# Optimization experiments

Hardware: AMD Instinct MI355X
Metric: run time of the kernel (lower is better)

Reference implementation:

```python
import jax, jax.numpy as jnp
import numpy as np
from jax import lax

B, N, IN_DIM = 8, 196, 2048
C = 256          # conv_channels / subspace dim
G = 1            # relation_glimpse


def _dilated_conv(x, w, b, dil):
    # x: [B,N,N,Cin], w: [3,3,Cin,Cout], SAME padding, rhs dilation per source
    y = lax.conv_general_dilated(x, w, window_strides=(1, 1), padding='SAME',
                                 rhs_dilation=dil,
                                 dimension_numbers=('NHWC', 'HWIO', 'NHWC'))
    return y + b


def _rel_map(X):
    # X: [B,N,N,G] -> symmetric add, move glimpse to axis 1, softmax over N*N
    Xs = X + jnp.transpose(X, (0, 2, 1, 3))          # [B,N,N,G]
    m = jnp.transpose(Xs, (0, 3, 2, 1))              # [B,G,N,N]
    bsz, g, n, _ = m.shape
    m = jax.nn.softmax(m.reshape(bsz, g, n * n), axis=2)
    return m.reshape(bsz, g, n, n)


def setup_inputs() -> dict:
    key = jax.random.key(0)
    ks = jax.random.split(key, 8)
    s = lambda *sh: 1.0 / np.sqrt(sh[-2] if len(sh) > 1 else sh[0])
    return {
        'x': jax.random.normal(ks[0], (B, N, IN_DIM), jnp.float32),
        'w_prj': jax.random.normal(ks[1], (IN_DIM, C), jnp.float32) * 0.02,
        'b_prj': jnp.zeros((C,), jnp.float32),
        'w01': jax.random.normal(ks[2], (C, C // 2), jnp.float32) * 0.06,
        'b01': jnp.zeros((C // 2,), jnp.float32),
        'w02': jax.random.normal(ks[3], (C // 2, C // 4), jnp.float32) * 0.09,
        'b02': jnp.zeros((C // 4,), jnp.float32),
        'w03': jax.random.normal(ks[4], (C // 4, G), jnp.float32) * 0.125,
        'b03': jnp.zeros((G,), jnp.float32),
        'w1': jax.random.normal(ks[5], (3, 3, C, C // 2), jnp.float32) * 0.02,
        'b1': jnp.zeros((C // 2,), jnp.float32),
        'w2': jax.random.normal(ks[6], (3, 3, C // 2, C // 4), jnp.float32) * 0.03,
        'b2': jnp.zeros((C // 4,), jnp.float32),
        'w3': jax.random.normal(ks[7], (3, 3, C // 4, G), jnp.float32) * 0.04,
        'b3': jnp.zeros((G,), jnp.float32),
    }


def reference(x, w_prj, b_prj, w01, b01, w02, b02, w03, b03,
              w1, b1, w2, b2, w3, b3):
    # project to subspace: [B,N,C]
    sub = jnp.einsum('bnd,dc->bnc', x, w_prj) + b_prj
    # pairwise outer product: pair[b,i,j,c] = sub[b,i,c]*sub[b,j,c]
    pair = sub[:, :, None, :] * sub[:, None, :, :]          # [B,N,N,C]

    # branch 0: stacked 1x1 convs (pointwise) with relu; dropout = identity (eval)
    X0 = jax.nn.relu(jnp.einsum('bijc,cd->bijd', pair, w01) + b01)
    X0 = jax.nn.relu(jnp.einsum('bijc,cd->bijd', X0, w02) + b02)
    X0 = jax.nn.relu(jnp.einsum('bijc,cd->bijd', X0, w03) + b03)  # [B,N,N,G]
    rel_map0 = _rel_map(X0)                                  # [B,G,N,N]

    # branch 1: stacked 3x3 dilated convs, dilations (1,1),(1,2),(1,4)
    X1 = jax.nn.relu(_dilated_conv(pair, w1, b1, (1, 1)))
    X1 = jax.nn.relu(_dilated_conv(X1, w2, b2, (1, 2)))
    X1 = jax.nn.relu(_dilated_conv(X1, w3, b3, (1, 4)))      # [B,N,N,G]
    rel_map1 = _rel_map(X1)

    # aggregation over glimpses: rel_x = sum_g (map1[g]@x + map0[g]@x) / (2G)
    rel_x = (jnp.einsum('bgij,bjd->bid', rel_map1, x) +
             jnp.einsum('bgij,bjd->bid', rel_map0, x)) / (2.0 * G)
    return rel_x.reshape(x.shape[0], -1)                     # [B, N*in_dim]
```

## Files before the change

kernel.cpp:

```cpp
#include <hip/hip_runtime.h>
#include <cmath>

#define N_TOK 196
#define NPX   38416
#define CDIM  256

typedef _Float16 f16;
typedef __attribute__((ext_vector_type(8))) _Float16 half8;
typedef __attribute__((ext_vector_type(4))) float f32x4;

__global__ __launch_bounds__(256) void gemm_splitk(
    const float* __restrict__ A, const float* __restrict__ B,
    float* __restrict__ P)
{
    __shared__ float As[16][68];
    __shared__ float Bs[16][68];
    int tid = threadIdx.x;
    int tx = tid & 15, ty = tid >> 4;
    int m0 = blockIdx.y * 64, n0 = blockIdx.x * 64;
    int kz = blockIdx.z;
    float acc[4][4] = {};
    for (int k0 = kz * 256; k0 < kz * 256 + 256; k0 += 16) {
        __syncthreads();
        for (int e = tid; e < 1024; e += 256) {
            int m = e >> 4, kk = e & 15;
            int gm = m0 + m;
            As[kk][m] = (gm < 1568) ? A[(size_t)gm * 2048 + k0 + kk] : 0.f;
        }
        for (int e = tid; e < 1024; e += 256) {
            int kk = e >> 6, n = e & 63;
            Bs[kk][n] = B[(size_t)(k0 + kk) * 256 + n0 + n];
        }
        __syncthreads();
        #pragma unroll
        for (int kk = 0; kk < 16; ++kk) {
            float4 av = *(const float4*)&As[kk][ty * 4];
            float4 bv = *(const float4*)&Bs[kk][tx * 4];
            float a[4] = {av.x, av.y, av.z, av.w};
            float b[4] = {bv.x, bv.y, bv.z, bv.w};
            #pragma unroll
            for (int u = 0; u < 4; ++u)
                #pragma unroll
                for (int v = 0; v < 4; ++v) acc[u][v] += a[u] * b[v];
        }
    }
    float* Pz = P + (size_t)kz * 401408;
    #pragma unroll
    for (int u = 0; u < 4; ++u) {
        int gm = m0 + ty * 4 + u;
        if (gm >= 1568) continue;
        #pragma unroll
        for (int v = 0; v < 4; ++v) {
            int gn = n0 + tx * 4 + v;
            Pz[(size_t)gm * 256 + gn] = acc[u][v];
        }
    }
}

__global__ void reduce_subh(const float* __restrict__ P,
                            const float* __restrict__ bias,
                            f16* __restrict__ subh)
{
    int e = blockIdx.x * 256 + threadIdx.x;
    if (e >= 401408) return;
    float s = bias[e & 255];
    #pragma unroll
    for (int z = 0; z < 8; ++z) s += P[(size_t)z * 401408 + e];
    subh[e] = (f16)s;
}

__global__ void cvt_wt(const float* __restrict__ w, f16* __restrict__ wt,
                       int Kc, int D, int total)
{
    int e = blockIdx.x * 256 + threadIdx.x;
    if (e >= total) return;
    int td = Kc * D;
    int tap = e / td, r = e - tap * td;
    int c = r / D, d = r - c * D;
    wt[(size_t)(tap * D + d) * Kc + c] = (f16)w[e];
}

__global__ void cvt_wfrag(const float* __restrict__ w, f16* __restrict__ wf,
                          int Kc, int D, int taps)
{
    int tiles = D >> 4, kch = Kc >> 5;
    int total = taps * tiles * kch * 64;
    int e = blockIdx.x * 256 + threadIdx.x;
    if (e >= total) return;
    int lane = e & 63;
    int rest = e >> 6;
    int k = rest % kch; rest /= kch;
    int tile = rest % tiles;
    int tap = rest / tiles;
    int l16 = lane & 15, quad = lane >> 4;
    const float* src = w + ((size_t)tap * Kc + k * 32 + quad * 8) * D + tile * 16 + l16;
    f16* dst = wf + (size_t)e * 8;
    #pragma unroll
    for (int j = 0; j < 8; ++j) dst[j] = (f16)src[(size_t)j * D];
}

__global__ __launch_bounds__(256) void cvt_xT(const float* __restrict__ x,
                                              f16* __restrict__ xht)
{
    __shared__ float t[32][33];
    int b = blockIdx.z;
    int i0 = blockIdx.y * 32, n0 = blockIdx.x * 32;
    const float* xb = x + (size_t)b * 196 * 2048;
    for (int e = threadIdx.x; e < 1024; e += 256) {
        int r = e >> 5, c = e & 31;
        int gi = i0 + r;
        t[r][c] = (gi < 196) ? xb[(size_t)gi * 2048 + n0 + c] : 0.f;
    }
    __syncthreads();
    f16* xb2 = xht + (size_t)b * 2048 * 200;
    for (int e = threadIdx.x; e < 1024; e += 256) {
        int nl = e >> 5, il = e & 31;
        int gi = i0 + il, gn = n0 + nl;
        if (gi < 200) xb2[(size_t)gn * 200 + gi] = (f16)t[il][nl];
    }
}

__global__ __launch_bounds__(256, 2) void conv1_mfma(
    const f16* __restrict__ sub_h,
    const f16* __restrict__ w1f,
    const float* __restrict__ b1,
    f16* __restrict__ Y1h)
{
    __shared__ f16 sh[17408];
    f16* SJ = sh;
    f16* SI = sh + 8976;
    f16* OT = sh;

    int b = blockIdx.z;
    int i0 = blockIdx.y * 8, j0 = blockIdx.x * 32;
    int tid = threadIdx.x;
    const f16* subB = sub_h + (size_t)b * N_TOK * CDIM;

    uint4 zz = make_uint4(0, 0, 0, 0);
    for (int e = tid; e < 1088; e += 256) {
        int r = e >> 5, q = e & 31;
        int gj = j0 - 1 + r;
        uint4 v = zz;
        if (gj >= 0 && gj < N_TOK) v = *(const uint4*)(subB + gj * CDIM + q * 8);
        *(uint4*)(SJ + r * 264 + q * 8) = v;
    }
    for (int e = tid; e < 320; e += 256) {
        int r = e >> 5, q = e & 31;
        int gi = i0 - 1 + r;
        uint4 v = zz;
        if (gi >= 0 && gi < N_TOK) v = *(const uint4*)(subB + gi * CDIM + q * 8);
        *(uint4*)(SI + r * 264 + q * 8) = v;
    }
    __syncthreads();

    int wave = tid >> 6, lane = tid & 63;
    int quad = lane >> 4, l16 = lane & 15;
    int p  = wave >> 1;
    int dh = wave & 1;
    int d0 = dh * 64;

    float bias_r[4];
    #pragma unroll
    for (int n = 0; n < 4; ++n) bias_r[n] = b1[d0 + n * 16 + l16];

    const f16* wbase = w1f + (size_t)lane * 8 + (size_t)dh * 4 * 4096;

    f32x4 zero = {0.f, 0.f, 0.f, 0.f};
    f32x4 acc[8][4];
    #pragma unroll
    for (int m = 0; m < 8; ++m)
        #pragma unroll
        for (int n = 0; n < 4; ++n) acc[m][n] = zero;

    for (int k = 0; k < 8; ++k) {
        int c0 = k * 32;
        half8 si[6];
        #pragma unroll
        for (int r = 0; r < 6; ++r)
            si[r] = *(const half8*)(SI + (p * 4 + r) * 264 + c0 + quad * 8);
        half8 sj[2][3];
        #pragma unroll
        for (int jf = 0; jf < 2; ++jf)
            #pragma unroll
            for (int dd = 0; dd < 3; ++dd)
                sj[jf][dd] = *(const half8*)(SJ + (jf * 16 + l16 + dd) * 264 + c0 + quad * 8);

        #pragma unroll
        for (int dj = 0; dj < 3; ++dj) {
            half8 bf[3][4];
            #pragma unroll
            for (int di = 0; di < 3; ++di)
                #pragma unroll
                for (int n = 0; n < 4; ++n)
                    bf[di][n] = *(const half8*)(wbase + (size_t)(di * 3 + dj) * 32768
                                                + n * 4096 + k * 512);
            #pragma unroll
            for (int r = 0; r < 6; ++r) {
                half8 a0 = si[r] * sj[0][dj];
                half8 a1 = si[r] * sj[1][dj];
                #pragma unroll
                for (int di = 0; di < 3; ++di) {
                    int i = r - di;
                    if (i < 0 || i > 3) continue;
                    #pragma unroll
                    for (int n = 0; n < 4; ++n) {
                        acc[i * 2 + 0][n] = __builtin_amdgcn_mfma_f32_16x16x32_f16(
                            a0, bf[di][n], acc[i * 2 + 0][n], 0, 0, 0);
                        acc[i * 2 + 1][n] = __builtin_amdgcn_mfma_f32_16x16x32_f16(
                            a1, bf[di][n], acc[i * 2 + 1][n], 0, 0, 0);
                    }
                }
            }
        }
    }

    __syncthreads();
    f16* Yb = Y1h + (size_t)b * NPX * 128;
    #pragma unroll
    for (int ph = 0; ph < 2; ++ph) {
        if (p == ph) {
            #pragma unroll
            for (int i = 0; i < 4; ++i)
                #pragma unroll
                for (int jf = 0; jf < 2; ++jf) {
                    int m = i * 2 + jf;
                    #pragma unroll
                    for (int n = 0; n < 4; ++n) {
                        int dl = d0 + n * 16 + l16;
                        #pragma unroll
                        for (int r = 0; r < 4; ++r) {
                            int pxl = i * 32 + jf * 16 + quad * 4 + r;
                            OT[pxl * 136 + dl] = (f16)fmaxf(acc[m][n][r] + bias_r[n], 0.f);
                        }
                    }
                }
        }
        __syncthreads();
        for (int e = tid; e < 2048; e += 256) {
            int pxl = e >> 4, q = e & 15;
            int gi = i0 + ph * 4 + (pxl >> 5), gj = j0 + (pxl & 31);
            if (gi < N_TOK && gj < N_TOK)
                *(uint4*)(Yb + ((size_t)gi * N_TOK + gj) * 128 + q * 8) =
                    *(const uint4*)(OT + pxl * 136 + q * 8);
        }
        __syncthreads();
    }
}

__global__ __launch_bounds__(256, 2) void conv2_mfma(
    const f16* __restrict__ Y1h, const f16* __restrict__ w2f,
    const float* __restrict__ b2, f16* __restrict__ Y2h)
{
    __shared__ f16 sh[19584];
    f16* Ys = sh;
    f16* OT = sh;

    int b = blockIdx.z;
    int i0 = blockIdx.y * 2, j0 = blockIdx.x * 32;
    int tid = threadIdx.x;
    const f16* Yb = Y1h + (size_t)b * NPX * 128;

    uint4 zz = make_uint4(0, 0, 0, 0);
    for (int e = tid; e < 2304; e += 256) {
        int ir = e / 576, rem = e - ir * 576;
        int jq = rem >> 4, q = rem & 15;
        int gi = i0 - 1 + ir, gj = j0 - 2 + jq;
        uint4 v = zz;
        if (gi >= 0 && gi < N_TOK && gj >= 0 && gj < N_TOK)
            v = *(const uint4*)(Yb + ((size_t)gi * N_TOK + gj) * 128 + q * 8);
        *(uint4*)(Ys + (ir * 36 + jq) * 136 + q * 8) = v;
    }
    __syncthreads();

    int wave = tid >> 6, lane = tid & 63;
    int quad = lane >> 4, l16 = lane & 15;
    int ii = wave >> 1, jb = (wave & 1) * 16;

    const f16* wbase = w2f + (size_t)lane * 8;

    f32x4 zero = {0.f, 0.f, 0.f, 0.f};
    f32x4 acc[4] = {zero, zero, zero, zero};

    #pragma unroll
    for (int tap = 0; tap < 9; ++tap) {
        int di = tap / 3 - 1, dj2 = (tap % 3 - 1) * 2;
        #pragma unroll
        for (int k = 0; k < 4; ++k) {
            int c0 = k * 32;
            half8 a = *(const half8*)(Ys + ((ii + di + 1) * 36 + jb + l16 + dj2 + 2) * 136
                                      + c0 + quad * 8);
            #pragma unroll
            for (int n = 0; n < 4; ++n) {
                half8 bf = *(const half8*)(wbase + (size_t)tap * 8192 + n * 2048 + k * 512);
                acc[n] = __builtin_amdgcn_mfma_f32_16x16x32_f16(a, bf, acc[n], 0, 0, 0);
            }
        }
    }
    __syncthreads();
    #pragma unroll
    for (int n = 0; n < 4; ++n) {
        int d = n * 16 + l16;
        float bias = b2[d];
        #pragma unroll
        for (int r = 0; r < 4; ++r) {
            int px = ii * 32 + jb + quad * 4 + r;
            OT[px * 72 + d] = (f16)fmaxf(acc[n][r] + bias, 0.f);
        }
    }
    __syncthreads();
    f16* Zb = Y2h + (size_t)b * NPX * 64;
    for (int e = tid; e < 512; e += 256) {
        int px = e >> 3, q = e & 7;
        int i = i0 + (px >> 5), j = j0 + (px & 31);
        if (j < N_TOK)
            *(uint4*)(Zb + ((size_t)i * N_TOK + j) * 64 + q * 8) =
                *(const uint4*)(OT + px * 72 + q * 8);
    }
}

__global__ __launch_bounds__(256) void conv3_h(
    const f16* __restrict__ Y2h, const float* __restrict__ w3,
    const float* __restrict__ b3, float* __restrict__ X1)
{
    __shared__ float w[576];
    int b = blockIdx.y;
    const f16* Yb = Y2h + (size_t)b * NPX * 64;
    for (int e = threadIdx.x; e < 576; e += 256) w[e] = w3[e];
    __syncthreads();
    int px = blockIdx.x * 256 + threadIdx.x;
    if (px >= NPX) return;
    int i = px / 196, j = px - i * 196;
    float s = b3[0];
    for (int tap = 0; tap < 9; ++tap) {
        int gi = i + tap / 3 - 1, gj = j + (tap % 3 - 1) * 4;
        if (gi < 0 || gi >= N_TOK || gj < 0 || gj >= N_TOK) continue;
        const half8* src = (const half8*)(Yb + ((size_t)gi * N_TOK + gj) * 64);
        const float* wt = w + tap * 64;
        #pragma unroll
        for (int q = 0; q < 8; ++q) {
            half8 h = src[q];
            #pragma unroll
            for (int e = 0; e < 8; ++e) s += (float)h[e] * wt[q * 8 + e];
        }
    }
    X1[(size_t)b * NPX + px] = fmaxf(s, 0.f);
}

__global__ __launch_bounds__(256, 2) void branch0_mfma(
    const f16* __restrict__ sub_h,
    const f16* __restrict__ w01t,
    const float* __restrict__ b01,
    const f16* __restrict__ w02t,
    const float* __restrict__ b02,
    const float* __restrict__ w03, const float* __restrict__ b03,
    float* __restrict__ X0)
{
    __shared__ f16 sh[32000];
    __shared__ float W3s[64];
    f16* SJ = sh;
    f16* SI = sh + 8448;
    f16* BW = sh + 9472;
    f16* H1 = sh + 14592;
    f16* H2 = sh;

    int b = blockIdx.z;
    int i0 = blockIdx.y * 4, j0 = blockIdx.x * 32;
    int tid = threadIdx.x;
    const f16* subB = sub_h + (size_t)b * N_TOK * CDIM;

    uint4 zz = make_uint4(0, 0, 0, 0);
    for (int e = tid; e < 1024; e += 256) {
        int r = e >> 5, q = e & 31;
        int gj = j0 + r;
        uint4 v = zz;
        if (gj < N_TOK) v = *(const uint4*)(subB + gj * CDIM + q * 8);
        *(uint4*)(SJ + r * 264 + q * 8) = v;
    }
    if (tid < 128) {
        int r = tid >> 5, q = tid & 31;
        int gi = i0 + r;
        uint4 v = zz;
        if (gi < N_TOK) v = *(const uint4*)(subB + gi * CDIM + q * 8);
        *(uint4*)(SI + r * 256 + q * 8) = v;
    }
    if (tid < 64) W3s[tid] = w03[tid];

    int wave = tid >> 6, lane = tid & 63;
    int quad = lane >> 4, l16 = lane & 15;
    int ii = wave;

    f32x4 zero = {0.f, 0.f, 0.f, 0.f};
    f32x4 acc[2][8];
    #pragma unroll
    for (int t = 0; t < 2; ++t)
        #pragma unroll
        for (int n = 0; n < 8; ++n) acc[t][n] = zero;

    for (int c0 = 0; c0 < 256; c0 += 32) {
        __syncthreads();
        for (int e = tid; e < 512; e += 256) {
            int d = e >> 2, q = e & 3;
            *(uint4*)(BW + d * 40 + q * 8) =
                *(const uint4*)(w01t + (size_t)d * 256 + c0 + q * 8);
        }
        __syncthreads();
        half8 sib = *(const half8*)(SI + ii * 256 + c0 + quad * 8);
        half8 a0 = sib * *(const half8*)(SJ + l16 * 264 + c0 + quad * 8);
        half8 a1 = sib * *(const half8*)(SJ + (l16 + 16) * 264 + c0 + quad * 8);
        #pragma unroll
        for (int n = 0; n < 8; ++n) {
            half8 bf = *(const half8*)(BW + (n * 16 + l16) * 40 + quad * 8);
            acc[0][n] = __builtin_amdgcn_mfma_f32_16x16x32_f16(a0, bf, acc[0][n], 0, 0, 0);
            acc[1][n] = __builtin_amdgcn_mfma_f32_16x16x32_f16(a1, bf, acc[1][n], 0, 0, 0);
        }
    }
    #pragma unroll
    for (int t = 0; t < 2; ++t)
        #pragma unroll
        for (int n = 0; n < 8; ++n) {
            int d = n * 16 + l16;
            float bias = b01[d];
            #pragma unroll
            for (int r = 0; r < 4; ++r) {
                int px = ii * 32 + t * 16 + quad * 4 + r;
                H1[px * 136 + d] = (f16)fmaxf(acc[t][n][r] + bias, 0.f);
            }
        }

    f32x4 acc2[2][4];
    #pragma unroll
    for (int t = 0; t < 2; ++t)
        #pragma unroll
        for (int n = 0; n < 4; ++n) acc2[t][n] = zero;

    for (int c0 = 0; c0 < 128; c0 += 32) {
        __syncthreads();
        {
            int d = tid >> 2, q = tid & 3;
            if (d < 64)
                *(uint4*)(BW + d * 40 + q * 8) =
                    *(const uint4*)(w02t + (size_t)d * 128 + c0 + q * 8);
        }
        __syncthreads();
        half8 a0 = *(const half8*)(H1 + (ii * 32 + l16) * 136 + c0 + quad * 8);
        half8 a1 = *(const half8*)(H1 + (ii * 32 + 16 + l16) * 136 + c0 + quad * 8);
        #pragma unroll
        for (int n = 0; n < 4; ++n) {
            half8 bf = *(const half8*)(BW + (n * 16 + l16) * 40 + quad * 8);
            acc2[0][n] = __builtin_amdgcn_mfma_f32_16x16x32_f16(a0, bf, acc2[0][n], 0, 0, 0);
            acc2[1][n] = __builtin_amdgcn_mfma_f32_16x16x32_f16(a1, bf, acc2[1][n], 0, 0, 0);
        }
    }
    #pragma unroll
    for (int t = 0; t < 2; ++t)
        #pragma unroll
        for (int n = 0; n < 4; ++n) {
            int e = n * 16 + l16;
            float bias = b02[e];
            #pragma unroll
            for (int r = 0; r < 4; ++r) {
                int px = ii * 32 + t * 16 + quad * 4 + r;
                H2[px * 72 + e] = (f16)fmaxf(acc2[t][n][r] + bias, 0.f);
            }
        }
    __syncthreads();
    if (tid < 128) {
        int px = tid;
        float s = b03[0];
        const f16* h = H2 + px * 72;
        #pragma unroll 8
        for (int c = 0; c < 64; ++c) s += (float)h[c] * W3s[c];
        int i = i0 + (px >> 5), j = j0 + (px & 31);
        if (j < N_TOK)
            X0[(size_t)b * NPX + i * N_TOK + j] = fmaxf(s, 0.f);
    }
}

__global__ __launch_bounds__(1024) void symsoftmax(float* __restrict__ X0,
                                                   float* __restrict__ X1)
{
    __shared__ float red[32];
    __shared__ float red2[32];
    float* X = (blockIdx.y ? X1 : X0) + (long long)blockIdx.x * NPX;
    int tid = threadIdx.x;
    float v[38];
    float mx = -3.0e38f;
    #pragma unroll
    for (int p = 0; p < 38; ++p) {
        int e = tid + p * 1024;
        if (e < NPX) {
            int i = e / 196, j = e - i * 196;
            float t = X[e] + X[j * 196 + i];
            v[p] = t;
            mx = fmaxf(mx, t);
        } else v[p] = -3.0e38f;
    }
    #pragma unroll
    for (int off = 32; off > 0; off >>= 1) mx = fmaxf(mx, __shfl_xor(mx, off));
    if ((tid & 63) == 0) red[tid >> 6] = mx;
    __syncthreads();
    if (tid < 64) {
        float m = (tid < 16) ? red[tid] : -3.0e38f;
        #pragma unroll
        for (int off = 8; off > 0; off >>= 1) m = fmaxf(m, __shfl_xor(m, off));
        if (tid == 0) red[0] = m;
    }
    __syncthreads();
    mx = red[0];
    float s = 0.f;
    #pragma unroll
    for (int p = 0; p < 38; ++p) {
        int e = tid + p * 1024;
        float ex = (e < NPX) ? expf(v[p] - mx) : 0.f;
        v[p] = ex;
        s += ex;
    }
    #pragma unroll
    for (int off = 32; off > 0; off >>= 1) s += __shfl_xor(s, off);
    if ((tid & 63) == 0) red2[tid >> 6] = s;
    __syncthreads();
    if (tid < 64) {
        float m = (tid < 16) ? red2[tid] : 0.f;
        #pragma unroll
        for (int off = 8; off > 0; off >>= 1) m += __shfl_xor(m, off);
        if (tid == 0) red2[0] = m;
    }
    __syncthreads();
    float scale = 0.5f / red2[0];
    #pragma unroll
    for (int p = 0; p < 38; ++p) {
        int e = tid + p * 1024;
        if (e < NPX) X[e] = v[p] * scale;
    }
}

__global__ void combine_ph(const float* __restrict__ X0,
                           const float* __restrict__ X1,
                           f16* __restrict__ Ph)
{
    int e = blockIdx.x * 256 + threadIdx.x;
    if (e >= 8 * 196 * 200) return;
    int j = e % 200;
    int row = e / 200;
    f16 v = (f16)0.f;
    if (j < 196) {
        int src = row * 196 + j;
        v = (f16)((X0[src] + X1[src]) * 512.0f);
    }
    Ph[e] = v;
}

__global__ __launch_bounds__(256, 2) void gemm_out(
    const f16* __restrict__ Ph, const f16* __restrict__ xht,
    float* __restrict__ out)
{
    __shared__ f16 As[64 * 72];
    __shared__ f16 Bs[128 * 72];
    int b = blockIdx.z;
    int n0 = blockIdx.x * 128, m0 = blockIdx.y * 64;
    int tid = threadIdx.x;
    const f16* Pb = Ph + (size_t)b * 196 * 200;
    const f16* xb = xht + (size_t)b * 2048 * 200;

    int wave = tid >> 6, lane = tid & 63;
    int quad = lane >> 4, l16 = lane & 15;

    f32x4 zero = {0.f, 0.f, 0.f, 0.f};
    f32x4 acc[8];
    #pragma unroll
    for (int n = 0; n < 8; ++n) acc[n] = zero;

    uint4 zz = make_uint4(0, 0, 0, 0);
    for (int k0 = 0; k0 < 256; k0 += 64) {
        __syncthreads();
        for (int e = tid; e < 512; e += 256) {
            int r = e >> 3, q = e & 7;
            int gm = m0 + r, k = k0 + q * 8;
            uint4 v = zz;
            if (gm < 196 && k < 200) v = *(const uint4*)(Pb + (size_t)gm * 200 + k);
            *(uint4*)(As + r * 72 + q * 8) = v;
        }
        for (int e = tid; e < 1024; e += 256) {
            int r = e >> 3, q = e & 7;
            int k = k0 + q * 8;
            uint4 v = zz;
            if (k < 200) v = *(const uint4*)(xb + (size_t)(n0 + r) * 200 + k);
            *(uint4*)(Bs + r * 72 + q * 8) = v;
        }
        __syncthreads();
        #pragma unroll
        for (int ks = 0; ks < 2; ++ks) {
            half8 a = *(const half8*)(As + (wave * 16 + l16) * 72 + ks * 32 + quad * 8);
            #pragma unroll
            for (int n = 0; n < 8; ++n) {
                half8 bf = *(const half8*)(Bs + (n * 16 + l16) * 72 + ks * 32 + quad * 8);
                acc[n] = __builtin_amdgcn_mfma_f32_16x16x32_f16(a, bf, acc[n], 0, 0, 0);
            }
        }
    }
    int m_base = m0 + wave * 16 + quad * 4;
    float* ob = out + (size_t)b * 196 * 2048;
    #pragma unroll
    for (int n = 0; n < 8; ++n) {
        int gn = n0 + n * 16 + l16;
        #pragma unroll
        for (int r = 0; r < 4; ++r) {
            int gm = m_base + r;
            if (gm < 196) ob[(size_t)gm * 2048 + gn] = acc[n][r] * (1.0f / 512.0f);
        }
    }
}

extern "C" void kernel_launch(void* const* d_in, const int* in_sizes, int n_in,
                              void* d_out, int out_size, void* d_ws, size_t ws_size,
                              hipStream_t stream)
{
    (void)in_sizes; (void)n_in; (void)out_size; (void)ws_size;
    const float* x     = (const float*)d_in[0];
    const float* w_prj = (const float*)d_in[1];
    const float* b_prj = (const float*)d_in[2];
    const float* w01   = (const float*)d_in[3];
    const float* b01   = (const float*)d_in[4];
    const float* w02   = (const float*)d_in[5];
    const float* b02   = (const float*)d_in[6];
    const float* w03   = (const float*)d_in[7];
    const float* b03   = (const float*)d_in[8];
    const float* w1    = (const float*)d_in[9];
    const float* b1    = (const float*)d_in[10];
    const float* w2    = (const float*)d_in[11];
    const float* b2    = (const float*)d_in[12];
    const float* w3    = (const float*)d_in[13];
    const float* b3    = (const float*)d_in[14];

    char* W = (char*)d_ws;
    float* part = (float*)(W + 0);
    float* X0   = (float*)(W + 12845056);
    float* X1   = (float*)(W + 14074368);
    f16*   subh = (f16*)(W + 15303680);
    f16*   w1f  = (f16*)(W + 16106496);
    f16*   w2f  = (f16*)(W + 16696320);
    f16*   w01t = (f16*)(W + 16843776);
    f16*   w02t = (f16*)(W + 16909312);
    f16*   Ph   = (f16*)(W + 16925696);
    f16*   xht  = (f16*)(W + 17552896);
    f16*   Y1h  = (f16*)(W + 24106496);
    f16*   Y2h  = (f16*)(W + 102782464);

    gemm_splitk<<<dim3(4, 25, 8), 256, 0, stream>>>(x, w_prj, part);
    reduce_subh<<<dim3(1568), 256, 0, stream>>>(part, b_prj, subh);

    cvt_wfrag<<<dim3(144), 256, 0, stream>>>(w1, w1f, 256, 128, 9);
    cvt_wfrag<<<dim3(36),  256, 0, stream>>>(w2, w2f, 128, 64, 9);
    cvt_wt<<<dim3(128),  256, 0, stream>>>(w01, w01t, 256, 128, 32768);
    cvt_wt<<<dim3(32),   256, 0, stream>>>(w02, w02t, 128, 64, 8192);
    cvt_xT<<<dim3(64, 7, 8), 256, 0, stream>>>(x, xht);

    branch0_mfma<<<dim3(7, 49, 8), 256, 0, stream>>>(
        subh, w01t, b01, w02t, b02, w03, b03, X0);

    conv1_mfma<<<dim3(7, 25, 8), 256, 0, stream>>>(subh, w1f, b1, Y1h);
    conv2_mfma<<<dim3(7, 98, 8), 256, 0, stream>>>(Y1h, w2f, b2, Y2h);
    conv3_h<<<dim3(151, 8), 256, 0, stream>>>(Y2h, w3, b3, X1);

    symsoftmax<<<dim3(8, 2), 1024, 0, stream>>>(X0, X1);

    combine_ph<<<dim3(1225), 256, 0, stream>>>(X0, X1, Ph);

    gemm_out<<<dim3(16, 4, 8), 256, 0, stream>>>(Ph, xht, (float*)d_out);
}
```

Baseline: 564.2 us.

## Shrink conv1 tile to 4 rows, load branch0 weights from pre-swizzled global fragments

conv1 now computes 4 output rows per block instead of 8, which halves the accumulator registers and allows 3 blocks per CU, with the grid doubled to 49 row-blocks. Each tap now recomputes the outer-product A fragments, so some of the SI reuse across taps is lost. branch0 drops its per-k-chunk LDS staging of transposed weights and the two __syncthreads per chunk. Instead it reads MFMA-fragment-ordered weights produced by cvt_wfrag directly from global/L2, and conv2's launch bound is raised to 4 blocks per CU.

```diff
diff --git a/kernel.cpp b/kernel.cpp
--- a/kernel.cpp
+++ b/kernel.cpp
@@ -69,17 +69,6 @@
     subh[e] = (f16)s;
 }
 
-__global__ void cvt_wt(const float* __restrict__ w, f16* __restrict__ wt,
-                       int Kc, int D, int total)
-{
-    int e = blockIdx.x * 256 + threadIdx.x;
-    if (e >= total) return;
-    int td = Kc * D;
-    int tap = e / td, r = e - tap * td;
-    int c = r / D, d = r - c * D;
-    wt[(size_t)(tap * D + d) * Kc + c] = (f16)w[e];
-}
-
 __global__ void cvt_wfrag(const float* __restrict__ w, f16* __restrict__ wf,
                           int Kc, int D, int taps)
 {
@@ -120,7 +109,7 @@
     }
 }
 
-__global__ __launch_bounds__(256, 2) void conv1_mfma(
+__global__ __launch_bounds__(256, 3) void conv1_mfma(
     const f16* __restrict__ sub_h,
     const f16* __restrict__ w1f,
     const float* __restrict__ b1,
@@ -132,7 +121,7 @@
     f16* OT = sh;
 
     int b = blockIdx.z;
-    int i0 = blockIdx.y * 8, j0 = blockIdx.x * 32;
+    int i0 = blockIdx.y * 4, j0 = blockIdx.x * 32;
     int tid = threadIdx.x;
     const f16* subB = sub_h + (size_t)b * N_TOK * CDIM;
 
@@ -144,8 +133,8 @@
         if (gj >= 0 && gj < N_TOK) v = *(const uint4*)(subB + gj * CDIM + q * 8);
         *(uint4*)(SJ + r * 264 + q * 8) = v;
     }
-    for (int e = tid; e < 320; e += 256) {
-        int r = e >> 5, q = e & 31;
+    if (tid < 192) {
+        int r = tid >> 5, q = tid & 31;
         int gi = i0 - 1 + r;
         uint4 v = zz;
         if (gi >= 0 && gi < N_TOK) v = *(const uint4*)(subB + gi * CDIM + q * 8);
@@ -166,88 +155,65 @@
     const f16* wbase = w1f + (size_t)lane * 8 + (size_t)dh * 4 * 4096;
 
     f32x4 zero = {0.f, 0.f, 0.f, 0.f};
-    f32x4 acc[8][4];
-    #pragma unroll
-    for (int m = 0; m < 8; ++m)
+    f32x4 acc[4][4];
+    #pragma unroll
+    for (int m = 0; m < 4; ++m)
         #pragma unroll
         for (int n = 0; n < 4; ++n) acc[m][n] = zero;
 
     for (int k = 0; k < 8; ++k) {
         int c0 = k * 32;
-        half8 si[6];
-        #pragma unroll
-        for (int r = 0; r < 6; ++r)
-            si[r] = *(const half8*)(SI + (p * 4 + r) * 264 + c0 + quad * 8);
-        half8 sj[2][3];
-        #pragma unroll
-        for (int jf = 0; jf < 2; ++jf)
-            #pragma unroll
-            for (int dd = 0; dd < 3; ++dd)
-                sj[jf][dd] = *(const half8*)(SJ + (jf * 16 + l16 + dd) * 264 + c0 + quad * 8);
-
-        #pragma unroll
-        for (int dj = 0; dj < 3; ++dj) {
-            half8 bf[3][4];
-            #pragma unroll
-            for (int di = 0; di < 3; ++di)
+        #pragma unroll
+        for (int tap = 0; tap < 9; ++tap) {
+            int di = tap / 3, dj = tap % 3;
+            half8 bf[4];
+            #pragma unroll
+            for (int n = 0; n < 4; ++n)
+                bf[n] = *(const half8*)(wbase + (size_t)tap * 32768 + n * 4096 + k * 512);
+            half8 si0 = *(const half8*)(SI + (p * 2 + 0 + di) * 264 + c0 + quad * 8);
+            half8 si1 = *(const half8*)(SI + (p * 2 + 1 + di) * 264 + c0 + quad * 8);
+            half8 sj0 = *(const half8*)(SJ + (l16 + dj) * 264 + c0 + quad * 8);
+            half8 sj1 = *(const half8*)(SJ + (l16 + 16 + dj) * 264 + c0 + quad * 8);
+            half8 a00 = si0 * sj0, a01 = si0 * sj1;
+            half8 a10 = si1 * sj0, a11 = si1 * sj1;
+            #pragma unroll
+            for (int n = 0; n < 4; ++n) {
+                acc[0][n] = __builtin_amdgcn_mfma_f32_16x16x32_f16(a00, bf[n], acc[0][n], 0, 0, 0);
+                acc[1][n] = __builtin_amdgcn_mfma_f32_16x16x32_f16(a01, bf[n], acc[1][n], 0, 0, 0);
+                acc[2][n] = __builtin_amdgcn_mfma_f32_16x16x32_f16(a10, bf[n], acc[2][n], 0, 0, 0);
+                acc[3][n] = __builtin_amdgcn_mfma_f32_16x16x32_f16(a11, bf[n], acc[3][n], 0, 0, 0);
+            }
+        }
+    }
+
+    __syncthreads();
+    #pragma unroll
+    for (int i = 0; i < 2; ++i)
+        #pragma unroll
+        for (int jf = 0; jf < 2; ++jf) {
+            int m = i * 2 + jf;
+            #pragma unroll
+            for (int n = 0; n < 4; ++n) {
+                int dl = d0 + n * 16 + l16;
                 #pragma unroll
-                for (int n = 0; n < 4; ++n)
-                    bf[di][n] = *(const half8*)(wbase + (size_t)(di * 3 + dj) * 32768
-                                                + n * 4096 + k * 512);
-            #pragma unroll
-            for (int r = 0; r < 6; ++r) {
-                half8 a0 = si[r] * sj[0][dj];
-                half8 a1 = si[r] * sj[1][dj];
-                #pragma unroll
-                for (int di = 0; di < 3; ++di) {
-                    int i = r - di;
-                    if (i < 0 || i > 3) continue;
-                    #pragma unroll
-                    for (int n = 0; n < 4; ++n) {
-                        acc[i * 2 + 0][n] = __builtin_amdgcn_mfma_f32_16x16x32_f16(
-                            a0, bf[di][n], acc[i * 2 + 0][n], 0, 0, 0);
-                        acc[i * 2 + 1][n] = __builtin_amdgcn_mfma_f32_16x16x32_f16(
-                            a1, bf[di][n], acc[i * 2 + 1][n], 0, 0, 0);
-                    }
+                for (int r = 0; r < 4; ++r) {
+                    int pxl = (p * 2 + i) * 32 + jf * 16 + quad * 4 + r;
+                    OT[pxl * 136 + dl] = (f16)fmaxf(acc[m][n][r] + bias_r[n], 0.f);
                 }
             }
         }
-    }
-
     __syncthreads();
     f16* Yb = Y1h + (size_t)b * NPX * 128;
-    #pragma unroll
-    for (int ph = 0; ph < 2; ++ph) {
-        if (p == ph) {
-            #pragma unroll
-            for (int i = 0; i < 4; ++i)
-                #pragma unroll
-                for (int jf = 0; jf < 2; ++jf) {
-                    int m = i * 2 + jf;
-                    #pragma unroll
-                    for (int n = 0; n < 4; ++n) {
-                        int dl = d0 + n * 16 + l16;
-                        #pragma unroll
-                        for (int r = 0; r < 4; ++r) {
-                            int pxl = i * 32 + jf * 16 + quad * 4 + r;
-                            OT[pxl * 136 + dl] = (f16)fmaxf(acc[m][n][r] + bias_r[n], 0.f);
-                        }
-                    }
-                }
-        }
-        __syncthreads();
-        for (int e = tid; e < 2048; e += 256) {
-            int pxl = e >> 4, q = e & 15;
-            int gi = i0 + ph * 4 + (pxl >> 5), gj = j0 + (pxl & 31);
-            if (gi < N_TOK && gj < N_TOK)
-                *(uint4*)(Yb + ((size_t)gi * N_TOK + gj) * 128 + q * 8) =
-                    *(const uint4*)(OT + pxl * 136 + q * 8);
-        }
-        __syncthreads();
-    }
-}
-
-__global__ __launch_bounds__(256, 2) void conv2_mfma(
+    for (int e = tid; e < 2048; e += 256) {
+        int pxl = e >> 4, q = e & 15;
+        int gi = i0 + (pxl >> 5), gj = j0 + (pxl & 31);
+        if (gj < N_TOK)
+            *(uint4*)(Yb + ((size_t)gi * N_TOK + gj) * 128 + q * 8) =
+                *(const uint4*)(OT + pxl * 136 + q * 8);
+    }
+}
+
+__global__ __launch_bounds__(256, 4) void conv2_mfma(
     const f16* __restrict__ Y1h, const f16* __restrict__ w2f,
     const float* __restrict__ b2, f16* __restrict__ Y2h)
 {
@@ -348,19 +314,18 @@
 
 __global__ __launch_bounds__(256, 2) void branch0_mfma(
     const f16* __restrict__ sub_h,
-    const f16* __restrict__ w01t,
+    const f16* __restrict__ w01f,
     const float* __restrict__ b01,
-    const f16* __restrict__ w02t,
+    const f16* __restrict__ w02f,
     const float* __restrict__ b02,
     const float* __restrict__ w03, const float* __restrict__ b03,
     float* __restrict__ X0)
 {
-    __shared__ f16 sh[32000];
+    __shared__ f16 sh[26912];
     __shared__ float W3s[64];
     f16* SJ = sh;
     f16* SI = sh + 8448;
-    f16* BW = sh + 9472;
-    f16* H1 = sh + 14592;
+    f16* H1 = sh + 9504;
     f16* H2 = sh;
 
     int b = blockIdx.z;
@@ -381,14 +346,18 @@
         int gi = i0 + r;
         uint4 v = zz;
         if (gi < N_TOK) v = *(const uint4*)(subB + gi * CDIM + q * 8);
-        *(uint4*)(SI + r * 256 + q * 8) = v;
+        *(uint4*)(SI + r * 264 + q * 8) = v;
     }
     if (tid < 64) W3s[tid] = w03[tid];
+    __syncthreads();
 
     int wave = tid >> 6, lane = tid & 63;
     int quad = lane >> 4, l16 = lane & 15;
     int ii = wave;
 
+    const f16* w1base = w01f + (size_t)lane * 8;
+    const f16* w2base = w02f + (size_t)lane * 8;
+
     f32x4 zero = {0.f, 0.f, 0.f, 0.f};
     f32x4 acc[2][8];
     #pragma unroll
@@ -396,20 +365,14 @@
         #pragma unroll
         for (int n = 0; n < 8; ++n) acc[t][n] = zero;
 
-    for (int c0 = 0; c0 < 256; c0 += 32) {
-        __syncthreads();
-        for (int e = tid; e < 512; e += 256) {
-            int d = e >> 2, q = e & 3;
-            *(uint4*)(BW + d * 40 + q * 8) =
-                *(const uint4*)(w01t + (size_t)d * 256 + c0 + q * 8);
-        }
-        __syncthreads();
-        half8 sib = *(const half8*)(SI + ii * 256 + c0 + quad * 8);
+    for (int k = 0; k < 8; ++k) {
+        int c0 = k * 32;
+        half8 sib = *(const half8*)(SI + ii * 264 + c0 + quad * 8);
         half8 a0 = sib * *(const half8*)(SJ + l16 * 264 + c0 + quad * 8);
         half8 a1 = sib * *(const half8*)(SJ + (l16 + 16) * 264 + c0 + quad * 8);
         #pragma unroll
         for (int n = 0; n < 8; ++n) {
-            half8 bf = *(const half8*)(BW + (n * 16 + l16) * 40 + quad * 8);
+            half8 bf = *(const half8*)(w1base + (size_t)n * 4096 + k * 512);
             acc[0][n] = __builtin_amdgcn_mfma_f32_16x16x32_f16(a0, bf, acc[0][n], 0, 0, 0);
             acc[1][n] = __builtin_amdgcn_mfma_f32_16x16x32_f16(a1, bf, acc[1][n], 0, 0, 0);
         }
@@ -426,6 +389,7 @@
                 H1[px * 136 + d] = (f16)fmaxf(acc[t][n][r] + bias, 0.f);
             }
         }
+    __syncthreads();
 
     f32x4 acc2[2][4];
     #pragma unroll
@@ -433,20 +397,13 @@
         #pragma unroll
         for (int n = 0; n < 4; ++n) acc2[t][n] = zero;
 
-    for (int c0 = 0; c0 < 128; c0 += 32) {
-        __syncthreads();
-        {
-            int d = tid >> 2, q = tid & 3;
-            if (d < 64)
-                *(uint4*)(BW + d * 40 + q * 8) =
-                    *(const uint4*)(w02t + (size_t)d * 128 + c0 + q * 8);
-        }
-        __syncthreads();
+    for (int k = 0; k < 4; ++k) {
+        int c0 = k * 32;
         half8 a0 = *(const half8*)(H1 + (ii * 32 + l16) * 136 + c0 + quad * 8);
         half8 a1 = *(const half8*)(H1 + (ii * 32 + 16 + l16) * 136 + c0 + quad * 8);
         #pragma unroll
         for (int n = 0; n < 4; ++n) {
-            half8 bf = *(const half8*)(BW + (n * 16 + l16) * 40 + quad * 8);
+            half8 bf = *(const half8*)(w2base + (size_t)n * 2048 + k * 512);
             acc2[0][n] = __builtin_amdgcn_mfma_f32_16x16x32_f16(a0, bf, acc2[0][n], 0, 0, 0);
             acc2[1][n] = __builtin_amdgcn_mfma_f32_16x16x32_f16(a1, bf, acc2[1][n], 0, 0, 0);
         }
@@ -639,8 +596,8 @@
     f16*   subh = (f16*)(W + 15303680);
     f16*   w1f  = (f16*)(W + 16106496);
     f16*   w2f  = (f16*)(W + 16696320);
-    f16*   w01t = (f16*)(W + 16843776);
-    f16*   w02t = (f16*)(W + 16909312);
+    f16*   w01f = (f16*)(W + 16843776);
+    f16*   w02f = (f16*)(W + 16909312);
     f16*   Ph   = (f16*)(W + 16925696);
     f16*   xht  = (f16*)(W + 17552896);
     f16*   Y1h  = (f16*)(W + 24106496);
@@ -651,14 +608,14 @@
 
     cvt_wfrag<<<dim3(144), 256, 0, stream>>>(w1, w1f, 256, 128, 9);
     cvt_wfrag<<<dim3(36),  256, 0, stream>>>(w2, w2f, 128, 64, 9);
-    cvt_wt<<<dim3(128),  256, 0, stream>>>(w01, w01t, 256, 128, 32768);
-    cvt_wt<<<dim3(32),   256, 0, stream>>>(w02, w02t, 128, 64, 8192);
+    cvt_wfrag<<<dim3(16),  256, 0, stream>>>(w01, w01f, 256, 128, 1);
+    cvt_wfrag<<<dim3(4),   256, 0, stream>>>(w02, w02f, 128, 64, 1);
     cvt_xT<<<dim3(64, 7, 8), 256, 0, stream>>>(x, xht);
 
     branch0_mfma<<<dim3(7, 49, 8), 256, 0, stream>>>(
-        subh, w01t, b01, w02t, b02, w03, b03, X0);
-
-    conv1_mfma<<<dim3(7, 25, 8), 256, 0, stream>>>(subh, w1f, b1, Y1h);
+        subh, w01f, b01, w02f, b02, w03, b03, X0);
+
+    conv1_mfma<<<dim3(7, 49, 8), 256, 0, stream>>>(subh, w1f, b1, Y1h);
     conv2_mfma<<<dim3(7, 98, 8), 256, 0, stream>>>(Y1h, w2f, b2, Y2h);
     conv3_h<<<dim3(151, 8), 256, 0, stream>>>(Y2h, w3, b3, X1);
 
```

After: 602.5 us. 6.8% more time.

## Shrink conv1 tile to 4 rows, split output channels across waves, double-buffer weights

Applied to the files above, without the earlier changes.

conv1 now gives each block 4 output rows instead of 8. Each of the four waves owns 32 output channels instead of splitting rows and channel halves between wave pairs. The grid grows to 49 row-blocks, and launch bounds allow 3 blocks per CU. Weight fragments are loaded per tap with a two-slot register double buffer, which lowers register pressure and lets more waves stay resident, at the cost of more redundant halo loads of the subspace rows. The output staging now takes a single pass, and the row bound check is dropped because 49*4 covers 196 exactly.

```diff
diff --git a/kernel.cpp b/kernel.cpp
--- a/kernel.cpp
+++ b/kernel.cpp
@@ -120,7 +120,7 @@
     }
 }
 
-__global__ __launch_bounds__(256, 2) void conv1_mfma(
+__global__ __launch_bounds__(256, 3) void conv1_mfma(
     const f16* __restrict__ sub_h,
     const f16* __restrict__ w1f,
     const float* __restrict__ b1,
@@ -132,7 +132,7 @@
     f16* OT = sh;
 
     int b = blockIdx.z;
-    int i0 = blockIdx.y * 8, j0 = blockIdx.x * 32;
+    int i0 = blockIdx.y * 4, j0 = blockIdx.x * 32;
     int tid = threadIdx.x;
     const f16* subB = sub_h + (size_t)b * N_TOK * CDIM;
 
@@ -144,8 +144,8 @@
         if (gj >= 0 && gj < N_TOK) v = *(const uint4*)(subB + gj * CDIM + q * 8);
         *(uint4*)(SJ + r * 264 + q * 8) = v;
     }
-    for (int e = tid; e < 320; e += 256) {
-        int r = e >> 5, q = e & 31;
+    if (tid < 192) {
+        int r = tid >> 5, q = tid & 31;
         int gi = i0 - 1 + r;
         uint4 v = zz;
         if (gi >= 0 && gi < N_TOK) v = *(const uint4*)(subB + gi * CDIM + q * 8);
@@ -155,29 +155,26 @@
 
     int wave = tid >> 6, lane = tid & 63;
     int quad = lane >> 4, l16 = lane & 15;
-    int p  = wave >> 1;
-    int dh = wave & 1;
-    int d0 = dh * 64;
-
-    float bias_r[4];
-    #pragma unroll
-    for (int n = 0; n < 4; ++n) bias_r[n] = b1[d0 + n * 16 + l16];
-
-    const f16* wbase = w1f + (size_t)lane * 8 + (size_t)dh * 4 * 4096;
+    int dh = wave;
+    int d0 = dh * 32;
+
+    float bias_r[2] = {b1[d0 + l16], b1[d0 + 16 + l16]};
+
+    const f16* wbase = w1f + (size_t)lane * 8 + (size_t)(2 * dh) * 4096;
 
     f32x4 zero = {0.f, 0.f, 0.f, 0.f};
-    f32x4 acc[8][4];
+    f32x4 acc[8][2];
     #pragma unroll
     for (int m = 0; m < 8; ++m)
         #pragma unroll
-        for (int n = 0; n < 4; ++n) acc[m][n] = zero;
+        for (int n = 0; n < 2; ++n) acc[m][n] = zero;
 
     for (int k = 0; k < 8; ++k) {
         int c0 = k * 32;
         half8 si[6];
         #pragma unroll
         for (int r = 0; r < 6; ++r)
-            si[r] = *(const half8*)(SI + (p * 4 + r) * 264 + c0 + quad * 8);
+            si[r] = *(const half8*)(SI + r * 264 + c0 + quad * 8);
         half8 sj[2][3];
         #pragma unroll
         for (int jf = 0; jf < 2; ++jf)
@@ -185,65 +182,56 @@
             for (int dd = 0; dd < 3; ++dd)
                 sj[jf][dd] = *(const half8*)(SJ + (jf * 16 + l16 + dd) * 264 + c0 + quad * 8);
 
-        #pragma unroll
-        for (int dj = 0; dj < 3; ++dj) {
-            half8 bf[3][4];
-            #pragma unroll
-            for (int di = 0; di < 3; ++di)
+        half8 bf[2][2];
+        #pragma unroll
+        for (int n = 0; n < 2; ++n)
+            bf[0][n] = *(const half8*)(wbase + (size_t)n * 4096 + k * 512);
+
+        #pragma unroll
+        for (int tap = 0; tap < 9; ++tap) {
+            int cur = tap & 1;
+            if (tap < 8) {
                 #pragma unroll
-                for (int n = 0; n < 4; ++n)
-                    bf[di][n] = *(const half8*)(wbase + (size_t)(di * 3 + dj) * 32768
-                                                + n * 4096 + k * 512);
-            #pragma unroll
-            for (int r = 0; r < 6; ++r) {
-                half8 a0 = si[r] * sj[0][dj];
-                half8 a1 = si[r] * sj[1][dj];
+                for (int n = 0; n < 2; ++n)
+                    bf[cur ^ 1][n] = *(const half8*)(wbase + (size_t)(tap + 1) * 32768
+                                                     + n * 4096 + k * 512);
+            }
+            int di = tap / 3, dj = tap % 3;
+            #pragma unroll
+            for (int i = 0; i < 4; ++i) {
+                half8 a0 = si[i + di] * sj[0][dj];
+                half8 a1 = si[i + di] * sj[1][dj];
                 #pragma unroll
-                for (int di = 0; di < 3; ++di) {
-                    int i = r - di;
-                    if (i < 0 || i > 3) continue;
-                    #pragma unroll
-                    for (int n = 0; n < 4; ++n) {
-                        acc[i * 2 + 0][n] = __builtin_amdgcn_mfma_f32_16x16x32_f16(
-                            a0, bf[di][n], acc[i * 2 + 0][n], 0, 0, 0);
-                        acc[i * 2 + 1][n] = __builtin_amdgcn_mfma_f32_16x16x32_f16(
-                            a1, bf[di][n], acc[i * 2 + 1][n], 0, 0, 0);
-                    }
+                for (int n = 0; n < 2; ++n) {
+                    acc[i * 2 + 0][n] = __builtin_amdgcn_mfma_f32_16x16x32_f16(
+                        a0, bf[cur][n], acc[i * 2 + 0][n], 0, 0, 0);
+                    acc[i * 2 + 1][n] = __builtin_amdgcn_mfma_f32_16x16x32_f16(
+                        a1, bf[cur][n], acc[i * 2 + 1][n], 0, 0, 0);
                 }
             }
         }
     }
 
     __syncthreads();
+    #pragma unroll
+    for (int m = 0; m < 8; ++m) {
+        int ib = (m >> 1) * 32 + (m & 1) * 16 + quad * 4;
+        #pragma unroll
+        for (int n = 0; n < 2; ++n) {
+            int dl = d0 + n * 16 + l16;
+            #pragma unroll
+            for (int r = 0; r < 4; ++r)
+                OT[(ib + r) * 136 + dl] = (f16)fmaxf(acc[m][n][r] + bias_r[n], 0.f);
+        }
+    }
+    __syncthreads();
     f16* Yb = Y1h + (size_t)b * NPX * 128;
-    #pragma unroll
-    for (int ph = 0; ph < 2; ++ph) {
-        if (p == ph) {
-            #pragma unroll
-            for (int i = 0; i < 4; ++i)
-                #pragma unroll
-                for (int jf = 0; jf < 2; ++jf) {
-                    int m = i * 2 + jf;
-                    #pragma unroll
-                    for (int n = 0; n < 4; ++n) {
-                        int dl = d0 + n * 16 + l16;
-                        #pragma unroll
-                        for (int r = 0; r < 4; ++r) {
-                            int pxl = i * 32 + jf * 16 + quad * 4 + r;
-                            OT[pxl * 136 + dl] = (f16)fmaxf(acc[m][n][r] + bias_r[n], 0.f);
-                        }
-                    }
-                }
-        }
-        __syncthreads();
-        for (int e = tid; e < 2048; e += 256) {
-            int pxl = e >> 4, q = e & 15;
-            int gi = i0 + ph * 4 + (pxl >> 5), gj = j0 + (pxl & 31);
-            if (gi < N_TOK && gj < N_TOK)
-                *(uint4*)(Yb + ((size_t)gi * N_TOK + gj) * 128 + q * 8) =
-                    *(const uint4*)(OT + pxl * 136 + q * 8);
-        }
-        __syncthreads();
+    for (int e = tid; e < 2048; e += 256) {
+        int pxl = e >> 4, q = e & 15;
+        int gi = i0 + (pxl >> 5), gj = j0 + (pxl & 31);
+        if (gj < N_TOK)
+            *(uint4*)(Yb + ((size_t)gi * N_TOK + gj) * 128 + q * 8) =
+                *(const uint4*)(OT + pxl * 136 + q * 8);
     }
 }
 
@@ -658,7 +646,7 @@
     branch0_mfma<<<dim3(7, 49, 8), 256, 0, stream>>>(
         subh, w01t, b01, w02t, b02, w03, b03, X0);
 
-    conv1_mfma<<<dim3(7, 25, 8), 256, 0, stream>>>(subh, w1f, b1, Y1h);
+    conv1_mfma<<<dim3(7, 49, 8), 256, 0, stream>>>(subh, w1f, b1, Y1h);
     conv2_mfma<<<dim3(7, 98, 8), 256, 0, stream>>>(Y1h, w2f, b2, Y2h);
     conv3_h<<<dim3(151, 8), 256, 0, stream>>>(Y2h, w3, b3, X1);
 
```

After: 952.2 us. 68.8% more time.

## Use f16 MFMA for projection GEMM and merge weight-conversion kernels

Applied to the files above, without the earlier changes.

The fp32 scalar-FMA split-K projection GEMM is rewritten to stage x and w_prj as f16 in shared memory and compute with 16x16x32 f16 MFMA instructions. The split factor drops from 8 to 4, so the reduction pass reads fewer partial buffers. The four weight-conversion launches are folded into one kernel to cut launch overhead. In exchange, the projection is now computed with f16 inputs, which lowers its precision, and the projection is only a small share of the total runtime.

```diff
diff --git a/kernel.cpp b/kernel.cpp
--- a/kernel.cpp
+++ b/kernel.cpp
@@ -9,50 +9,50 @@
 typedef __attribute__((ext_vector_type(8))) _Float16 half8;
 typedef __attribute__((ext_vector_type(4))) float f32x4;
 
-__global__ __launch_bounds__(256) void gemm_splitk(
-    const float* __restrict__ A, const float* __restrict__ B,
+__global__ __launch_bounds__(256) void gemm_prj(
+    const float* __restrict__ x,
+    const float* __restrict__ wp,
     float* __restrict__ P)
 {
-    __shared__ float As[16][68];
-    __shared__ float Bs[16][68];
+    __shared__ f16 As[64 * 40];
+    __shared__ f16 Bs[64 * 40];
     int tid = threadIdx.x;
-    int tx = tid & 15, ty = tid >> 4;
     int m0 = blockIdx.y * 64, n0 = blockIdx.x * 64;
     int kz = blockIdx.z;
-    float acc[4][4] = {};
-    for (int k0 = kz * 256; k0 < kz * 256 + 256; k0 += 16) {
-        __syncthreads();
-        for (int e = tid; e < 1024; e += 256) {
-            int m = e >> 4, kk = e & 15;
+    int wave = tid >> 6, lane = tid & 63;
+    int quad = lane >> 4, l16 = lane & 15;
+    f32x4 zero = {0.f, 0.f, 0.f, 0.f};
+    f32x4 acc[4] = {zero, zero, zero, zero};
+
+    for (int k0 = kz * 512; k0 < kz * 512 + 512; k0 += 32) {
+        __syncthreads();
+        for (int e = tid; e < 2048; e += 256) {
+            int m = e >> 5, kk = e & 31;
             int gm = m0 + m;
-            As[kk][m] = (gm < 1568) ? A[(size_t)gm * 2048 + k0 + kk] : 0.f;
-        }
-        for (int e = tid; e < 1024; e += 256) {
+            float v = (gm < 1568) ? x[(size_t)gm * 2048 + k0 + kk] : 0.f;
+            As[m * 40 + kk] = (f16)v;
+        }
+        for (int e = tid; e < 2048; e += 256) {
             int kk = e >> 6, n = e & 63;
-            Bs[kk][n] = B[(size_t)(k0 + kk) * 256 + n0 + n];
-        }
-        __syncthreads();
-        #pragma unroll
-        for (int kk = 0; kk < 16; ++kk) {
-            float4 av = *(const float4*)&As[kk][ty * 4];
-            float4 bv = *(const float4*)&Bs[kk][tx * 4];
-            float a[4] = {av.x, av.y, av.z, av.w};
-            float b[4] = {bv.x, bv.y, bv.z, bv.w};
-            #pragma unroll
-            for (int u = 0; u < 4; ++u)
-                #pragma unroll
-                for (int v = 0; v < 4; ++v) acc[u][v] += a[u] * b[v];
+            Bs[n * 40 + kk] = (f16)wp[(size_t)(k0 + kk) * 256 + n0 + n];
+        }
+        __syncthreads();
+        half8 a = *(const half8*)(As + (wave * 16 + l16) * 40 + quad * 8);
+        #pragma unroll
+        for (int nt = 0; nt < 4; ++nt) {
+            half8 bf = *(const half8*)(Bs + (nt * 16 + l16) * 40 + quad * 8);
+            acc[nt] = __builtin_amdgcn_mfma_f32_16x16x32_f16(a, bf, acc[nt], 0, 0, 0);
         }
     }
     float* Pz = P + (size_t)kz * 401408;
-    #pragma unroll
-    for (int u = 0; u < 4; ++u) {
-        int gm = m0 + ty * 4 + u;
-        if (gm >= 1568) continue;
-        #pragma unroll
-        for (int v = 0; v < 4; ++v) {
-            int gn = n0 + tx * 4 + v;
-            Pz[(size_t)gm * 256 + gn] = acc[u][v];
+    int mb = m0 + wave * 16 + quad * 4;
+    #pragma unroll
+    for (int nt = 0; nt < 4; ++nt) {
+        int gn = n0 + nt * 16 + l16;
+        #pragma unroll
+        for (int r = 0; r < 4; ++r) {
+            int gm = mb + r;
+            if (gm < 1568) Pz[(size_t)gm * 256 + gn] = acc[nt][r];
         }
     }
 }
@@ -65,28 +65,14 @@
     if (e >= 401408) return;
     float s = bias[e & 255];
     #pragma unroll
-    for (int z = 0; z < 8; ++z) s += P[(size_t)z * 401408 + e];
+    for (int z = 0; z < 4; ++z) s += P[(size_t)z * 401408 + e];
     subh[e] = (f16)s;
 }
 
-__global__ void cvt_wt(const float* __restrict__ w, f16* __restrict__ wt,
-                       int Kc, int D, int total)
-{
-    int e = blockIdx.x * 256 + threadIdx.x;
-    if (e >= total) return;
-    int td = Kc * D;
-    int tap = e / td, r = e - tap * td;
-    int c = r / D, d = r - c * D;
-    wt[(size_t)(tap * D + d) * Kc + c] = (f16)w[e];
-}
-
-__global__ void cvt_wfrag(const float* __restrict__ w, f16* __restrict__ wf,
-                          int Kc, int D, int taps)
+__device__ __forceinline__ void frag_pack(const float* w, f16* wf,
+                                          int Kc, int D, int e)
 {
     int tiles = D >> 4, kch = Kc >> 5;
-    int total = taps * tiles * kch * 64;
-    int e = blockIdx.x * 256 + threadIdx.x;
-    if (e >= total) return;
     int lane = e & 63;
     int rest = e >> 6;
     int k = rest % kch; rest /= kch;
@@ -97,6 +83,29 @@
     f16* dst = wf + (size_t)e * 8;
     #pragma unroll
     for (int j = 0; j < 8; ++j) dst[j] = (f16)src[(size_t)j * D];
+}
+
+__global__ void cvt_all(const float* __restrict__ w1, const float* __restrict__ w2,
+                        const float* __restrict__ w01, const float* __restrict__ w02,
+                        f16* __restrict__ w1f, f16* __restrict__ w2f,
+                        f16* __restrict__ w01t, f16* __restrict__ w02t)
+{
+    int blk = blockIdx.x, tid = threadIdx.x;
+    if (blk < 144) {
+        int e = blk * 256 + tid;
+        frag_pack(w1, w1f, 256, 128, e);
+    } else if (blk < 180) {
+        int e = (blk - 144) * 256 + tid;
+        frag_pack(w2, w2f, 128, 64, e);
+    } else if (blk < 308) {
+        int e = (blk - 180) * 256 + tid;
+        int c = e >> 7, d = e & 127;
+        w01t[(size_t)d * 256 + c] = (f16)w01[e];
+    } else {
+        int e = (blk - 308) * 256 + tid;
+        int c = e >> 6, d = e & 63;
+        w02t[(size_t)d * 128 + c] = (f16)w02[e];
+    }
 }
 
 __global__ __launch_bounds__(256) void cvt_xT(const float* __restrict__ x,
@@ -646,13 +655,10 @@
     f16*   Y1h  = (f16*)(W + 24106496);
     f16*   Y2h  = (f16*)(W + 102782464);
 
-    gemm_splitk<<<dim3(4, 25, 8), 256, 0, stream>>>(x, w_prj, part);
+    gemm_prj<<<dim3(4, 25, 4), 256, 0, stream>>>(x, w_prj, part);
     reduce_subh<<<dim3(1568), 256, 0, stream>>>(part, b_prj, subh);
 
-    cvt_wfrag<<<dim3(144), 256, 0, stream>>>(w1, w1f, 256, 128, 9);
-    cvt_wfrag<<<dim3(36),  256, 0, stream>>>(w2, w2f, 128, 64, 9);
-    cvt_wt<<<dim3(128),  256, 0, stream>>>(w01, w01t, 256, 128, 32768);
-    cvt_wt<<<dim3(32),   256, 0, stream>>>(w02, w02t, 128, 64, 8192);
+    cvt_all<<<dim3(340), 256, 0, stream>>>(w1, w2, w01, w02, w1f, w2f, w01t, w02t);
     cvt_xT<<<dim3(64, 7, 8), 256, 0, stream>>>(x, xht);
 
     branch0_mfma<<<dim3(7, 49, 8), 256, 0, stream>>>(
```

After: 569.0 us. Within noise of the previous version (+0.8%).
